# Optimization experiments

Measured on AMD Instinct MI355X. Metric: run time of the kernel, lower is better.

The kernel has to match this reference:

```python
import jax, jax.numpy as jnp
import numpy as np

VOCAB, EMB, ENC_H, DEC_H, ATTN = 32000, 512, 512, 1024, 512
B, S = 64, 128
ENC2 = 2 * ENC_H


def setup_inputs() -> dict:
    key = jax.random.key(0)
    ks = jax.random.split(key, 14)
    s = 0.02
    return {
        "input_token": jax.random.randint(ks[0], (B,), 0, VOCAB),
        "hidden": jax.random.normal(ks[1], (B, DEC_H), jnp.float32),
        "cell": jax.random.normal(ks[2], (B, DEC_H), jnp.float32),
        "encoder_outputs": jax.random.normal(ks[3], (S, B, ENC2), jnp.float32),
        "mask": jnp.ones((B, S), jnp.int32),
        "embedding": jax.random.normal(ks[4], (VOCAB, EMB), jnp.float32) * s,
        "W_enc": jax.random.normal(ks[5], (ATTN, ENC2), jnp.float32) * s,
        "W_dec": jax.random.normal(ks[6], (ATTN, DEC_H), jnp.float32) * s,
        "v_attn": jax.random.normal(ks[7], (ATTN,), jnp.float32) * s,
        "W_ih": jax.random.normal(ks[8], (4 * DEC_H, EMB + ENC2), jnp.float32) * s,
        "W_hh": jax.random.normal(ks[9], (4 * DEC_H, DEC_H), jnp.float32) * s,
        "b_ih": jnp.zeros((4 * DEC_H,), jnp.float32),
        "b_hh": jnp.zeros((4 * DEC_H,), jnp.float32),
        "W_out": jax.random.normal(ks[10], (VOCAB, DEC_H + ENC2 + EMB), jnp.float32) * s,
        "b_out": jnp.zeros((VOCAB,), jnp.float32),
    }


def reference(input_token, hidden, cell, encoder_outputs, mask,
              embedding, W_enc, W_dec, v_attn, W_ih, W_hh, b_ih, b_hh,
              W_out, b_out):
    # Embedding with padding_idx=0 (row 0 zeroed in torch; emulate by zeroing lookup)
    embedded = embedding[input_token]                                # [B, EMB]
    embedded = jnp.where((input_token == 0)[:, None], 0.0, embedded)
    # Dropout in eval mode -> identity

    # Bahdanau attention
    enc_proj = jnp.einsum('sbe,ae->sba', encoder_outputs, W_enc)      # [S, B, ATTN]
    dec_proj = hidden @ W_dec.T                                       # [B, ATTN]
    scores = jnp.einsum('sba,a->sb', jnp.tanh(enc_proj + dec_proj[None]), v_attn)
    scores = scores.T                                                 # [B, S]
    scores = jnp.where(mask == 0, -jnp.inf, scores)
    attn_w = jax.nn.softmax(scores, axis=1)                           # [B, S]
    context = jnp.einsum('bs,sbe->be', attn_w, encoder_outputs)       # [B, ENC2]

    # LSTMCell (torch gate order: i, f, g, o)
    x = jnp.concatenate([embedded, context], axis=1)                  # [B, EMB+ENC2]
    gates = x @ W_ih.T + b_ih + hidden @ W_hh.T + b_hh                # [B, 4*DEC_H]
    i, f, g, o = jnp.split(gates, 4, axis=1)
    i, f, o = jax.nn.sigmoid(i), jax.nn.sigmoid(f), jax.nn.sigmoid(o)
    g = jnp.tanh(g)
    new_cell = f * cell + i * g
    new_hidden = o * jnp.tanh(new_cell)

    # Output projection
    out_in = jnp.concatenate([new_hidden, context, embedded], axis=1)
    output = out_in @ W_out.T + b_out                                 # [B, VOCAB]
    return output, new_hidden, new_cell, attn_w
```

## Files before the change

### kernel.cpp

```cpp
#include <hip/hip_runtime.h>

#define VOCAB 32000
#define EMB   512
#define ENC2  1024
#define DECH  1024
#define ATTN  512
#define BB    64
#define SS    128
#define KXH   2560
#define KOI   2560

typedef __attribute__((ext_vector_type(4))) float  f32x4;
typedef __attribute__((ext_vector_type(8))) __bf16 bf16x8;

#define OFF_SC  0
#define OFF_CTX 32768
#define OFF_GP  294912
#define OFF_XH  4489216
#define OFF_OI  4816896
#define OFF_WE  5144576

static __device__ __forceinline__ bf16x8 cvt8(const float* p) {
    f32x4 a = *(const f32x4*)p;
    f32x4 b = *(const f32x4*)(p + 4);
    bf16x8 t;
    t[0] = (__bf16)a[0]; t[1] = (__bf16)a[1]; t[2] = (__bf16)a[2]; t[3] = (__bf16)a[3];
    t[4] = (__bf16)b[0]; t[5] = (__bf16)b[1]; t[6] = (__bf16)b[2]; t[7] = (__bf16)b[3];
    return t;
}

static __device__ __forceinline__ f32x4 mfma16(bf16x8 a, bf16x8 b, f32x4 c) {
    return __builtin_amdgcn_mfma_f32_16x16x32_bf16(a, b, c, 0, 0, 0);
}

__global__ __launch_bounds__(256) void k_init(const float* __restrict__ We,
                                              __bf16* __restrict__ we16,
                                              const int* __restrict__ tok,
                                              const float* __restrict__ hidden,
                                              const float* __restrict__ emb,
                                              __bf16* __restrict__ xh,
                                              __bf16* __restrict__ oi,
                                              const float* __restrict__ Wd,
                                              float* __restrict__ dp) {
    int bid = blockIdx.x, t = threadIdx.x;
    if (bid < 256) {
        int base = (bid * 256 + t) * 8;
        *(bf16x8*)(we16 + base) = cvt8(We + base);
    } else if (bid < 320) {
        int b = bid - 256;
        int tk = tok[b];
        #pragma unroll
        for (int j = 0; j < 2; ++j) {
            int e = t + 256 * j;
            float v = (tk == 0) ? 0.f : emb[tk * EMB + e];
            __bf16 h = (__bf16)v;
            xh[b * KXH + e] = h;
            oi[b * KOI + 2048 + e] = h;
        }
        #pragma unroll
        for (int j = 0; j < 4; ++j) {
            int hidx = t + 256 * j;
            xh[b * KXH + 1536 + hidx] = (__bf16)hidden[b * DECH + hidx];
        }
    } else {
        int bx = bid - 320;
        int w = t >> 6, l = t & 63, lo = l & 15, hi = l >> 4;
        int n = bx * 64 + w * 16 + lo;
        f32x4 acc[4];
        #pragma unroll
        for (int m = 0; m < 4; ++m) acc[m] = (f32x4){0.f, 0.f, 0.f, 0.f};
        for (int k0 = 0; k0 < DECH; k0 += 32) {
            int k = k0 + hi * 8;
            bf16x8 bf = cvt8(Wd + n * DECH + k);
            #pragma unroll
            for (int m = 0; m < 4; ++m) {
                bf16x8 af = cvt8(hidden + (m * 16 + lo) * DECH + k);
                acc[m] = mfma16(af, bf, acc[m]);
            }
        }
        #pragma unroll
        for (int m = 0; m < 4; ++m)
            #pragma unroll
            for (int ri = 0; ri < 4; ++ri) {
                int b = m * 16 + hi * 4 + ri;
                dp[b * ATTN + n] = acc[m][ri];
            }
    }
}

__global__ __launch_bounds__(256) void k_scores(const float* __restrict__ enc,
                                                const __bf16* __restrict__ we16,
                                                const float* __restrict__ dp,
                                                const float* __restrict__ v,
                                                float* __restrict__ sc) {
    int t = threadIdx.x;
    int w = t >> 6, l = t & 63, lo = l & 15, hi = l >> 4;
    int r0 = blockIdx.x * 32;
    int cb = w * 128;
    f32x4 acc[2][8];
    #pragma unroll
    for (int m = 0; m < 2; ++m)
        #pragma unroll
        for (int f = 0; f < 8; ++f) acc[m][f] = (f32x4){0.f, 0.f, 0.f, 0.f};

    const float* arow0 = enc + (r0 + lo) * ENC2 + hi * 8;
    const float* arow1 = enc + (r0 + 16 + lo) * ENC2 + hi * 8;
    for (int k0 = 0; k0 < ENC2; k0 += 32) {
        bf16x8 a0 = cvt8(arow0 + k0);
        bf16x8 a1 = cvt8(arow1 + k0);
        #pragma unroll
        for (int f = 0; f < 8; ++f) {
            bf16x8 bf = *(const bf16x8*)(we16 + (cb + f * 16 + lo) * ENC2 + k0 + hi * 8);
            acc[0][f] = mfma16(a0, bf, acc[0][f]);
            acc[1][f] = mfma16(a1, bf, acc[1][f]);
        }
    }
    int s_ = r0 >> 6;
    float p[2][4] = {{0.f,0.f,0.f,0.f},{0.f,0.f,0.f,0.f}};
    #pragma unroll
    for (int f = 0; f < 8; ++f) {
        int c = cb + f * 16 + lo;
        float vv = v[c];
        #pragma unroll
        for (int m = 0; m < 2; ++m)
            #pragma unroll
            for (int ri = 0; ri < 4; ++ri) {
                int r = r0 + m * 16 + hi * 4 + ri;
                int b = r & 63;
                p[m][ri] += vv * tanhf(acc[m][f][ri] + dp[b * ATTN + c]);
            }
    }
    #pragma unroll
    for (int x = 1; x < 16; x <<= 1) {
        #pragma unroll
        for (int m = 0; m < 2; ++m)
            #pragma unroll
            for (int ri = 0; ri < 4; ++ri) p[m][ri] += __shfl_xor(p[m][ri], x);
    }
    if (lo == 0) {
        #pragma unroll
        for (int m = 0; m < 2; ++m)
            #pragma unroll
            for (int ri = 0; ri < 4; ++ri) {
                int r = r0 + m * 16 + hi * 4 + ri;
                atomicAdd(&sc[(r & 63) * SS + s_], p[m][ri]);
            }
    }
}

__global__ void k_softmax(const float* __restrict__ sc, const int* __restrict__ mask,
                          float* __restrict__ attn) {
    int b = blockIdx.x, l = threadIdx.x;
    float s0 = sc[b * SS + l], s1 = sc[b * SS + 64 + l];
    if (mask[b * SS + l] == 0)      s0 = -3.0e38f;
    if (mask[b * SS + 64 + l] == 0) s1 = -3.0e38f;
    float m = fmaxf(s0, s1);
    #pragma unroll
    for (int x = 32; x >= 1; x >>= 1) m = fmaxf(m, __shfl_xor(m, x));
    float e0 = expf(s0 - m), e1 = expf(s1 - m);
    float sum = e0 + e1;
    #pragma unroll
    for (int x = 32; x >= 1; x >>= 1) sum += __shfl_xor(sum, x);
    float inv = 1.f / sum;
    attn[b * SS + l] = e0 * inv;
    attn[b * SS + 64 + l] = e1 * inv;
}

__global__ __launch_bounds__(256) void k_context(const float* __restrict__ enc,
                                                 const float* __restrict__ attn,
                                                 float* __restrict__ ctx) {
    int b = blockIdx.x & 63, sl = blockIdx.x >> 6, t = threadIdx.x;
    __shared__ float w[32];
    if (t < 32) w[t] = attn[b * SS + sl * 32 + t];
    __syncthreads();
    float acc[4] = {0.f, 0.f, 0.f, 0.f};
    for (int si = 0; si < 32; ++si) {
        int s = sl * 32 + si;
        float ws = w[si];
        const float* e = enc + (s * BB + b) * ENC2;
        #pragma unroll
        for (int j = 0; j < 4; ++j) acc[j] += ws * e[t + 256 * j];
    }
    #pragma unroll
    for (int j = 0; j < 4; ++j) atomicAdd(&ctx[b * ENC2 + t + 256 * j], acc[j]);
}

__global__ void k_ctxfin(const float* __restrict__ ctx,
                         __bf16* __restrict__ xh, __bf16* __restrict__ oi) {
    int b = blockIdx.x, t = threadIdx.x;
    #pragma unroll
    for (int j = 0; j < 4; ++j) {
        int e = t + 256 * j;
        __bf16 h = (__bf16)ctx[b * ENC2 + e];
        xh[b * KXH + 512 + e] = h;
        oi[b * KOI + 1024 + e] = h;
    }
}

__global__ __launch_bounds__(256) void k_gates(const __bf16* __restrict__ xh,
                                               const float* __restrict__ Wih,
                                               const float* __restrict__ Whh,
                                               float* __restrict__ gp) {
    int bx = blockIdx.x, ks = blockIdx.y;
    int t = threadIdx.x, w = t >> 6, l = t & 63, lo = l & 15, hi = l >> 4;
    int n = bx * 64 + w * 16 + lo;
    f32x4 acc[4];
    #pragma unroll
    for (int m = 0; m < 4; ++m) acc[m] = (f32x4){0.f, 0.f, 0.f, 0.f};
    int kend = ks * 640 + 640;
    for (int k0 = ks * 640; k0 < kend; k0 += 32) {
        int k = k0 + hi * 8;
        const float* bp = (k0 < 1536) ? (Wih + n * 1536 + k) : (Whh + n * 1024 + (k - 1536));
        bf16x8 bf = cvt8(bp);
        #pragma unroll
        for (int m = 0; m < 4; ++m) {
            bf16x8 af = *(const bf16x8*)(xh + (m * 16 + lo) * KXH + k);
            acc[m] = mfma16(af, bf, acc[m]);
        }
    }
    float* out = gp + ks * (BB * 4096);
    #pragma unroll
    for (int m = 0; m < 4; ++m)
        #pragma unroll
        for (int ri = 0; ri < 4; ++ri) {
            int row = m * 16 + hi * 4 + ri;
            out[row * 4096 + n] = acc[m][ri];
        }
}

__global__ void k_lstm(const float* __restrict__ gp, const float* __restrict__ bih,
                       const float* __restrict__ bhh, const float* __restrict__ cell,
                       float* __restrict__ nh_out, float* __restrict__ nc_out,
                       __bf16* __restrict__ oi) {
    int b = blockIdx.x, t = threadIdx.x;
    #pragma unroll
    for (int j = 0; j < 4; ++j) {
        int h = t + 256 * j;
        float gi = 0.f, gf = 0.f, gg = 0.f, go = 0.f;
        #pragma unroll
        for (int ks = 0; ks < 4; ++ks) {
            const float* g = gp + ks * (BB * 4096) + b * 4096;
            gi += g[h]; gf += g[1024 + h]; gg += g[2048 + h]; go += g[3072 + h];
        }
        gi += bih[h] + bhh[h];
        gf += bih[1024 + h] + bhh[1024 + h];
        gg += bih[2048 + h] + bhh[2048 + h];
        go += bih[3072 + h] + bhh[3072 + h];
        float i_ = 1.f / (1.f + expf(-gi));
        float f_ = 1.f / (1.f + expf(-gf));
        float o_ = 1.f / (1.f + expf(-go));
        float g_ = tanhf(gg);
        float nc = f_ * cell[b * DECH + h] + i_ * g_;
        float nh = o_ * tanhf(nc);
        nc_out[b * DECH + h] = nc;
        nh_out[b * DECH + h] = nh;
        oi[b * KOI + h] = (__bf16)nh;
    }
}

__global__ __launch_bounds__(256) void k_out(const __bf16* __restrict__ oi,
                                             const float* __restrict__ Wo,
                                             const float* __restrict__ bo,
                                             float* __restrict__ out) {
    int bx = blockIdx.x;
    int t = threadIdx.x, w = t >> 6, l = t & 63, lo = l & 15, hi = l >> 4;
    int n = bx * 64 + w * 16 + lo;
    f32x4 acc[4];
    #pragma unroll
    for (int m = 0; m < 4; ++m) acc[m] = (f32x4){0.f, 0.f, 0.f, 0.f};
    const float* wrow = Wo + (long)n * KOI;
    for (int k0 = 0; k0 < KOI; k0 += 32) {
        int k = k0 + hi * 8;
        bf16x8 bf = cvt8(wrow + k);
        #pragma unroll
        for (int m = 0; m < 4; ++m) {
            bf16x8 af = *(const bf16x8*)(oi + (m * 16 + lo) * KOI + k);
            acc[m] = mfma16(af, bf, acc[m]);
        }
    }
    float bb = bo[n];
    #pragma unroll
    for (int m = 0; m < 4; ++m)
        #pragma unroll
        for (int ri = 0; ri < 4; ++ri) {
            int row = m * 16 + hi * 4 + ri;
            out[row * VOCAB + n] = acc[m][ri] + bb;
        }
}

extern "C" void kernel_launch(void* const* d_in, const int* in_sizes, int n_in,
                              void* d_out, int out_size, void* d_ws, size_t ws_size,
                              hipStream_t stream) {
    const int*   tok    = (const int*)d_in[0];
    const float* hidden = (const float*)d_in[1];
    const float* cell   = (const float*)d_in[2];
    const float* enc    = (const float*)d_in[3];
    const int*   mask   = (const int*)d_in[4];
    const float* emb    = (const float*)d_in[5];
    const float* We     = (const float*)d_in[6];
    const float* Wd     = (const float*)d_in[7];
    const float* v      = (const float*)d_in[8];
    const float* Wih    = (const float*)d_in[9];
    const float* Whh    = (const float*)d_in[10];
    const float* bih    = (const float*)d_in[11];
    const float* bhh    = (const float*)d_in[12];
    const float* Wo     = (const float*)d_in[13];
    const float* bo     = (const float*)d_in[14];

    char* ws = (char*)d_ws;
    float*  sc   = (float*)(ws + OFF_SC);
    float*  ctx  = (float*)(ws + OFF_CTX);
    float*  gp   = (float*)(ws + OFF_GP);
    __bf16* xh   = (__bf16*)(ws + OFF_XH);
    __bf16* oi   = (__bf16*)(ws + OFF_OI);
    __bf16* we16 = (__bf16*)(ws + OFF_WE);
    float*  dp   = (float*)(ws + OFF_WE + 1048576);

    float* out_logits = (float*)d_out;
    float* nh   = out_logits + BB * VOCAB;
    float* nc   = nh + BB * DECH;
    float* attn = nc + BB * DECH;

    hipMemsetAsync(sc, 0, (BB * SS + BB * ENC2) * sizeof(float), stream);
    k_init<<<328, 256, 0, stream>>>(We, we16, tok, hidden, emb, xh, oi, Wd, dp);
    k_scores<<<256, 256, 0, stream>>>(enc, we16, dp, v, sc);
    k_softmax<<<BB, 64, 0, stream>>>(sc, mask, attn);
    k_context<<<256, 256, 0, stream>>>(enc, attn, ctx);
    k_ctxfin<<<BB, 256, 0, stream>>>(ctx, xh, oi);
    dim3 g2(64, 4);
    k_gates<<<g2, 256, 0, stream>>>(xh, Wih, Whh, gp);
    k_lstm<<<BB, 256, 0, stream>>>(gp, bih, bhh, cell, nh, nc, oi);
    k_out<<<500, 256, 0, stream>>>(oi, Wo, bo, out_logits);
}
```

Baseline: 683.8 us.

## Fuse softmax into context kernel, drop atomics and memset, defer context reduction

Scores are now reduced within each block through LDS and written directly instead of with atomicAdd, which removes the memset. Softmax is recomputed inside each context block, so the separate softmax launch goes away. Context partials are written per slice and summed on the fly where they are consumed: the gates GEMM sums and converts them, and the LSTM kernel writes them into the output-projection input. This removes the ctxfin kernel, and the gates GEMM reads hidden in fp32 directly. The cost is redundant softmax work in each block, extra partial-sum reads inside the gates GEMM inner loop, and a branch on k inside that loop.

```diff
diff --git a/kernel.cpp b/kernel.cpp
--- a/kernel.cpp
+++ b/kernel.cpp
@@ -13,12 +13,13 @@
 typedef __attribute__((ext_vector_type(4))) float  f32x4;
 typedef __attribute__((ext_vector_type(8))) __bf16 bf16x8;
 
-#define OFF_SC  0
-#define OFF_CTX 32768
-#define OFF_GP  294912
-#define OFF_XH  4489216
-#define OFF_OI  4816896
-#define OFF_WE  5144576
+#define OFF_SC   0
+#define OFF_CTXP 32768
+#define OFF_GP   1081344
+#define OFF_XE   5275648
+#define OFF_OI   5341184
+#define OFF_WE   5668864
+#define OFF_DP   6717440
 
 static __device__ __forceinline__ bf16x8 cvt8(const float* p) {
     f32x4 a = *(const f32x4*)p;
@@ -29,6 +30,18 @@
     return t;
 }
 
+static __device__ __forceinline__ bf16x8 sum4cvt(const float* p) {
+    f32x4 a = *(const f32x4*)p;
+    f32x4 b = *(const f32x4*)(p + 4);
+    a += *(const f32x4*)(p + 65536);  b += *(const f32x4*)(p + 65536 + 4);
+    a += *(const f32x4*)(p + 131072); b += *(const f32x4*)(p + 131072 + 4);
+    a += *(const f32x4*)(p + 196608); b += *(const f32x4*)(p + 196608 + 4);
+    bf16x8 t;
+    t[0] = (__bf16)a[0]; t[1] = (__bf16)a[1]; t[2] = (__bf16)a[2]; t[3] = (__bf16)a[3];
+    t[4] = (__bf16)b[0]; t[5] = (__bf16)b[1]; t[6] = (__bf16)b[2]; t[7] = (__bf16)b[3];
+    return t;
+}
+
 static __device__ __forceinline__ f32x4 mfma16(bf16x8 a, bf16x8 b, f32x4 c) {
     return __builtin_amdgcn_mfma_f32_16x16x32_bf16(a, b, c, 0, 0, 0);
 }
@@ -38,7 +51,7 @@
                                               const int* __restrict__ tok,
                                               const float* __restrict__ hidden,
                                               const float* __restrict__ emb,
-                                              __bf16* __restrict__ xh,
+                                              __bf16* __restrict__ xe,
                                               __bf16* __restrict__ oi,
                                               const float* __restrict__ Wd,
                                               float* __restrict__ dp) {
@@ -54,13 +67,8 @@
             int e = t + 256 * j;
             float v = (tk == 0) ? 0.f : emb[tk * EMB + e];
             __bf16 h = (__bf16)v;
-            xh[b * KXH + e] = h;
+            xe[b * EMB + e] = h;
             oi[b * KOI + 2048 + e] = h;
-        }
-        #pragma unroll
-        for (int j = 0; j < 4; ++j) {
-            int hidx = t + 256 * j;
-            xh[b * KXH + 1536 + hidx] = (__bf16)hidden[b * DECH + hidx];
         }
     } else {
         int bx = bid - 320;
@@ -97,6 +105,7 @@
     int w = t >> 6, l = t & 63, lo = l & 15, hi = l >> 4;
     int r0 = blockIdx.x * 32;
     int cb = w * 128;
+    __shared__ float lds_p[4][32];
     f32x4 acc[2][8];
     #pragma unroll
     for (int m = 0; m < 2; ++m)
@@ -115,7 +124,6 @@
             acc[1][f] = mfma16(a1, bf, acc[1][f]);
         }
     }
-    int s_ = r0 >> 6;
     float p[2][4] = {{0.f,0.f,0.f,0.f},{0.f,0.f,0.f,0.f}};
     #pragma unroll
     for (int f = 0; f < 8; ++f) {
@@ -125,8 +133,7 @@
         for (int m = 0; m < 2; ++m)
             #pragma unroll
             for (int ri = 0; ri < 4; ++ri) {
-                int r = r0 + m * 16 + hi * 4 + ri;
-                int b = r & 63;
+                int b = (r0 + m * 16 + hi * 4 + ri) & 63;
                 p[m][ri] += vv * tanhf(acc[m][f][ri] + dp[b * ATTN + c]);
             }
     }
@@ -141,63 +148,67 @@
         #pragma unroll
         for (int m = 0; m < 2; ++m)
             #pragma unroll
-            for (int ri = 0; ri < 4; ++ri) {
-                int r = r0 + m * 16 + hi * 4 + ri;
-                atomicAdd(&sc[(r & 63) * SS + s_], p[m][ri]);
-            }
-    }
-}
-
-__global__ void k_softmax(const float* __restrict__ sc, const int* __restrict__ mask,
-                          float* __restrict__ attn) {
-    int b = blockIdx.x, l = threadIdx.x;
-    float s0 = sc[b * SS + l], s1 = sc[b * SS + 64 + l];
-    if (mask[b * SS + l] == 0)      s0 = -3.0e38f;
-    if (mask[b * SS + 64 + l] == 0) s1 = -3.0e38f;
-    float m = fmaxf(s0, s1);
-    #pragma unroll
-    for (int x = 32; x >= 1; x >>= 1) m = fmaxf(m, __shfl_xor(m, x));
-    float e0 = expf(s0 - m), e1 = expf(s1 - m);
-    float sum = e0 + e1;
-    #pragma unroll
-    for (int x = 32; x >= 1; x >>= 1) sum += __shfl_xor(sum, x);
-    float inv = 1.f / sum;
-    attn[b * SS + l] = e0 * inv;
-    attn[b * SS + 64 + l] = e1 * inv;
-}
-
-__global__ __launch_bounds__(256) void k_context(const float* __restrict__ enc,
-                                                 const float* __restrict__ attn,
-                                                 float* __restrict__ ctx) {
+            for (int ri = 0; ri < 4; ++ri) lds_p[w][m * 16 + hi * 4 + ri] = p[m][ri];
+    }
+    __syncthreads();
+    if (t < 32) {
+        float s_ = lds_p[0][t] + lds_p[1][t] + lds_p[2][t] + lds_p[3][t];
+        int r = r0 + t;
+        sc[(r & 63) * SS + (r >> 6)] = s_;
+    }
+}
+
+__global__ __launch_bounds__(256) void k_ctx(const float* __restrict__ enc,
+                                             const float* __restrict__ sc,
+                                             const int* __restrict__ mask,
+                                             float* __restrict__ ctxp,
+                                             float* __restrict__ attn) {
     int b = blockIdx.x & 63, sl = blockIdx.x >> 6, t = threadIdx.x;
-    __shared__ float w[32];
-    if (t < 32) w[t] = attn[b * SS + sl * 32 + t];
+    __shared__ float ws_[SS];
+    __shared__ float red[4];
+    float val = 0.f, e = 0.f;
+    if (t < SS) {
+        val = sc[b * SS + t];
+        if (mask[b * SS + t] == 0) val = -3.0e38f;
+        float m = val;
+        #pragma unroll
+        for (int x = 32; x >= 1; x >>= 1) m = fmaxf(m, __shfl_xor(m, x));
+        if ((t & 63) == 0) red[t >> 6] = m;
+    }
     __syncthreads();
+    float M = fmaxf(red[0], red[1]);
+    if (t < SS) {
+        e = expf(val - M);
+        float s = e;
+        #pragma unroll
+        for (int x = 32; x >= 1; x >>= 1) s += __shfl_xor(s, x);
+        if ((t & 63) == 0) red[2 + (t >> 6)] = s;
+    }
+    __syncthreads();
+    float inv = 1.f / (red[2] + red[3]);
+    if (t < SS) {
+        float wv = e * inv;
+        ws_[t] = wv;
+        if (sl == 0) attn[b * SS + t] = wv;
+    }
+    __syncthreads();
+
     float acc[4] = {0.f, 0.f, 0.f, 0.f};
     for (int si = 0; si < 32; ++si) {
         int s = sl * 32 + si;
-        float ws = w[si];
-        const float* e = enc + (s * BB + b) * ENC2;
-        #pragma unroll
-        for (int j = 0; j < 4; ++j) acc[j] += ws * e[t + 256 * j];
-    }
-    #pragma unroll
-    for (int j = 0; j < 4; ++j) atomicAdd(&ctx[b * ENC2 + t + 256 * j], acc[j]);
-}
-
-__global__ void k_ctxfin(const float* __restrict__ ctx,
-                         __bf16* __restrict__ xh, __bf16* __restrict__ oi) {
-    int b = blockIdx.x, t = threadIdx.x;
-    #pragma unroll
-    for (int j = 0; j < 4; ++j) {
-        int e = t + 256 * j;
-        __bf16 h = (__bf16)ctx[b * ENC2 + e];
-        xh[b * KXH + 512 + e] = h;
-        oi[b * KOI + 1024 + e] = h;
-    }
-}
-
-__global__ __launch_bounds__(256) void k_gates(const __bf16* __restrict__ xh,
+        float wv = ws_[s];
+        const float* ep = enc + (s * BB + b) * ENC2;
+        #pragma unroll
+        for (int j = 0; j < 4; ++j) acc[j] += wv * ep[t + 256 * j];
+    }
+    float* outp = ctxp + (sl * 64 + b) * ENC2;
+    #pragma unroll
+    for (int j = 0; j < 4; ++j) outp[t + 256 * j] = acc[j];
+}
+
+__global__ __launch_bounds__(256) void k_gates(const __bf16* __restrict__ xe,
+                                               const float* __restrict__ ctxp,
+                                               const float* __restrict__ hidden,
                                                const float* __restrict__ Wih,
                                                const float* __restrict__ Whh,
                                                float* __restrict__ gp) {
@@ -214,7 +225,11 @@
         bf16x8 bf = cvt8(bp);
         #pragma unroll
         for (int m = 0; m < 4; ++m) {
-            bf16x8 af = *(const bf16x8*)(xh + (m * 16 + lo) * KXH + k);
+            int row = m * 16 + lo;
+            bf16x8 af;
+            if (k0 < 512)        af = *(const bf16x8*)(xe + row * EMB + k);
+            else if (k0 < 1536)  af = sum4cvt(ctxp + row * ENC2 + (k - 512));
+            else                 af = cvt8(hidden + row * DECH + (k - 1536));
             acc[m] = mfma16(af, bf, acc[m]);
         }
     }
@@ -230,6 +245,7 @@
 
 __global__ void k_lstm(const float* __restrict__ gp, const float* __restrict__ bih,
                        const float* __restrict__ bhh, const float* __restrict__ cell,
+                       const float* __restrict__ ctxp,
                        float* __restrict__ nh_out, float* __restrict__ nc_out,
                        __bf16* __restrict__ oi) {
     int b = blockIdx.x, t = threadIdx.x;
@@ -255,6 +271,9 @@
         nc_out[b * DECH + h] = nc;
         nh_out[b * DECH + h] = nh;
         oi[b * KOI + h] = (__bf16)nh;
+        float c4 = ctxp[b * ENC2 + h] + ctxp[65536 + b * ENC2 + h]
+                 + ctxp[131072 + b * ENC2 + h] + ctxp[196608 + b * ENC2 + h];
+        oi[b * KOI + 1024 + h] = (__bf16)c4;
     }
 }
 
@@ -309,26 +328,23 @@
 
     char* ws = (char*)d_ws;
     float*  sc   = (float*)(ws + OFF_SC);
-    float*  ctx  = (float*)(ws + OFF_CTX);
+    float*  ctxp = (float*)(ws + OFF_CTXP);
     float*  gp   = (float*)(ws + OFF_GP);
-    __bf16* xh   = (__bf16*)(ws + OFF_XH);
+    __bf16* xe   = (__bf16*)(ws + OFF_XE);
     __bf16* oi   = (__bf16*)(ws + OFF_OI);
     __bf16* we16 = (__bf16*)(ws + OFF_WE);
-    float*  dp   = (float*)(ws + OFF_WE + 1048576);
+    float*  dp   = (float*)(ws + OFF_DP);
 
     float* out_logits = (float*)d_out;
     float* nh   = out_logits + BB * VOCAB;
     float* nc   = nh + BB * DECH;
     float* attn = nc + BB * DECH;
 
-    hipMemsetAsync(sc, 0, (BB * SS + BB * ENC2) * sizeof(float), stream);
-    k_init<<<328, 256, 0, stream>>>(We, we16, tok, hidden, emb, xh, oi, Wd, dp);
+    k_init<<<328, 256, 0, stream>>>(We, we16, tok, hidden, emb, xe, oi, Wd, dp);
     k_scores<<<256, 256, 0, stream>>>(enc, we16, dp, v, sc);
-    k_softmax<<<BB, 64, 0, stream>>>(sc, mask, attn);
-    k_context<<<256, 256, 0, stream>>>(enc, attn, ctx);
-    k_ctxfin<<<BB, 256, 0, stream>>>(ctx, xh, oi);
+    k_ctx<<<256, 256, 0, stream>>>(enc, sc, mask, ctxp, attn);
     dim3 g2(64, 4);
-    k_gates<<<g2, 256, 0, stream>>>(xh, Wih, Whh, gp);
-    k_lstm<<<BB, 256, 0, stream>>>(gp, bih, bhh, cell, nh, nc, oi);
+    k_gates<<<g2, 256, 0, stream>>>(xe, ctxp, hidden, Wih, Whh, gp);
+    k_lstm<<<BB, 256, 0, stream>>>(gp, bih, bhh, cell, ctxp, nh, nc, oi);
     k_out<<<500, 256, 0, stream>>>(oi, Wo, bo, out_logits);
 }
```

After: 755.4 us. 10.5% more time.
